# Kernel optimization log

Hardware: AMD Instinct MI355X
Metric: run time of the kernel (lower is better)

## Reference

```python
import jax, jax.numpy as jnp
import numpy as np

OUT = 7           # pooled output size
SR = 2            # sampling_ratio
SCALES = (0.25, 0.125, 0.0625, 0.03125)
K_MIN = 2         # -log2(scales[0])
CANON_SCALE = 224.0
CANON_LVL = 4.0
EPS = 1e-6


def map_levels(boxes):
    # boxes: [N,4] in image coords -> level index in [0, 3]
    area = (boxes[:, 2] - boxes[:, 0]) * (boxes[:, 3] - boxes[:, 1])
    s = jnp.sqrt(area)
    lvl = jnp.floor(CANON_LVL + jnp.log2(s / CANON_SCALE + EPS))
    lvl = jnp.clip(lvl, K_MIN, K_MIN + len(SCALES) - 1)
    return lvl.astype(jnp.int32) - K_MIN


def _sample_coords(lo, bin_sz):
    # sample points within each of OUT bins, SR samples per bin -> [OUT*SR]
    grid = (jnp.arange(OUT, dtype=jnp.float32)[:, None] * bin_sz
            + (jnp.arange(SR, dtype=jnp.float32)[None, :] + 0.5) * bin_sz / SR)
    return lo + grid.reshape(-1)


def _roi_align_single(feat, img, box, scale):
    # feat: [B,C,H,W] (closed over batch under vmap), img: scalar int, box: [4]
    H, W = feat.shape[2], feat.shape[3]
    x1 = box[0] * scale
    y1 = box[1] * scale
    x2 = box[2] * scale
    y2 = box[3] * scale
    roi_w = jnp.maximum(x2 - x1, 1.0)
    roi_h = jnp.maximum(y2 - y1, 1.0)
    ys = _sample_coords(y1, roi_h / OUT)  # [14]
    xs = _sample_coords(x1, roi_w / OUT)  # [14]
    P = OUT * SR
    yg = jnp.broadcast_to(ys[:, None], (P, P)).reshape(-1)  # [196]
    xg = jnp.broadcast_to(xs[None, :], (P, P)).reshape(-1)  # [196]
    # ROIAlign CUDA semantics: out-of-range samples contribute 0
    valid = (yg >= -1.0) & (yg <= H) & (xg >= -1.0) & (xg <= W)
    y = jnp.clip(yg, 0.0, H - 1)
    x = jnp.clip(xg, 0.0, W - 1)
    y0 = jnp.floor(y).astype(jnp.int32)
    x0 = jnp.floor(x).astype(jnp.int32)
    y1i = jnp.minimum(y0 + 1, H - 1)
    x1i = jnp.minimum(x0 + 1, W - 1)
    ly = y - y0
    lx = x - x0
    hy = 1.0 - ly
    hx = 1.0 - lx
    # advanced indices (img, y, x) separated by ':' slice -> result [196, C]
    v00 = feat[img, :, y0, x0]
    v01 = feat[img, :, y0, x1i]
    v10 = feat[img, :, y1i, x0]
    v11 = feat[img, :, y1i, x1i]
    val = ((hy * hx)[:, None] * v00 + (hy * lx)[:, None] * v01
           + (ly * hx)[:, None] * v10 + (ly * lx)[:, None] * v11)
    val = jnp.where(valid[:, None], val, 0.0)
    # [196,C] -> [OUT,SR,OUT,SR,C] -> average over sampling grid -> [OUT,OUT,C]
    val = val.reshape(OUT, SR, OUT, SR, -1).mean(axis=(1, 3))
    return jnp.transpose(val, (2, 0, 1))  # [C,7,7]


def _pooler(feats, boxes, img_ids):
    levels = map_levels(boxes)  # [N]
    N = boxes.shape[0]
    C = feats[0].shape[1]
    result = jnp.zeros((N, C, OUT, OUT), dtype=feats[0].dtype)
    roi_align = jax.vmap(_roi_align_single, in_axes=(None, 0, 0, None))
    for lvl, (feat, scale) in enumerate(zip(feats, SCALES)):
        out_l = roi_align(feat, img_ids, boxes, scale)  # [N,C,7,7]
        result = jnp.where((levels == lvl)[:, None, None, None], out_l, result)
    return result


def setup_inputs() -> dict:
    key = jax.random.key(0)
    ks = jax.random.split(key, 7)
    B, C, N = 2, 256, 1000
    feat0 = jax.random.normal(ks[0], (B, C, 200, 200), jnp.float32)
    feat1 = jax.random.normal(ks[1], (B, C, 100, 100), jnp.float32)
    feat2 = jax.random.normal(ks[2], (B, C, 50, 50), jnp.float32)
    feat3 = jax.random.normal(ks[3], (B, C, 25, 25), jnp.float32)
    # log-uniform box sizes in [16, 400] px spread ROIs across all 4 levels
    wh = jnp.exp(jax.random.uniform(ks[4], (N, 2), minval=jnp.log(16.0),
                                    maxval=jnp.log(400.0)))
    xy = jax.random.uniform(ks[5], (N, 2)) * (800.0 - wh)
    boxes = jnp.concatenate([xy, xy + wh], axis=1)  # [N,4] x1,y1,x2,y2
    img_ids = jax.random.randint(ks[6], (N,), 0, B, dtype=jnp.int32)
    return {"feat0": feat0, "feat1": feat1, "feat2": feat2, "feat3": feat3,
            "boxes": boxes, "img_ids": img_ids}


def reference(feat0, feat1, feat2, feat3, boxes, img_ids):
    return _pooler((feat0, feat1, feat2, feat3), boxes, img_ids)
```

## Files before the change

### kernel.cpp

```cpp
#include <hip/hip_runtime.h>

#define OUTD 7
#define SRD 2
#define PD (OUTD * SRD)
#define NCH 256
#define CHUNK 32

__global__ __launch_bounds__(1024)
void sort_kernel(const float* __restrict__ boxes,
                 const int*   __restrict__ img_ids,
                 int* __restrict__ order, int N)
{
    __shared__ unsigned long long kv[1024];
    const int t = threadIdx.x;

    unsigned int key = 0xFFFFFFFFu;
    if (t < N) {
        const float bx1 = boxes[t * 4 + 0];
        const float by1 = boxes[t * 4 + 1];
        const float bx2 = boxes[t * 4 + 2];
        const float by2 = boxes[t * 4 + 3];
        const float area = (bx2 - bx1) * (by2 - by1);
        const float s = sqrtf(area);
        float lvlf = floorf(4.0f + log2f(s / 224.0f + 1e-6f));
        lvlf = fminf(fmaxf(lvlf, 2.0f), 5.0f);
        const int lvl = (int)lvlf - 2;
        const float scales[4] = {0.25f, 0.125f, 0.0625f, 0.03125f};
        const float sc = scales[lvl];
        int cx = (int)(0.5f * (bx1 + bx2) * sc);
        int cy = (int)(0.5f * (by1 + by2) * sc);
        cx = min(max(cx, 0), 127);
        cy = min(max(cy, 0), 127);
        unsigned int m = 0;
#pragma unroll
        for (int b = 0; b < 7; ++b)
            m |= ((cy >> b) & 1u) << (2 * b + 1) | ((cx >> b) & 1u) << (2 * b);
        key = ((((unsigned)lvl << 1) | (unsigned)img_ids[t]) << 14) | m;
    }
    kv[t] = ((unsigned long long)key << 32) | (unsigned)t;
    __syncthreads();

    for (int k = 2; k <= 1024; k <<= 1) {
        for (int j = k >> 1; j > 0; j >>= 1) {
            const int ixj = t ^ j;
            if (ixj > t) {
                const bool up = ((t & k) == 0);
                const unsigned long long a = kv[t], b = kv[ixj];
                if ((a > b) == up) { kv[t] = b; kv[ixj] = a; }
            }
            __syncthreads();
        }
    }
    if (t < N) order[t] = (int)(kv[t] & 0xFFFFFFFFu);
}

__global__ __launch_bounds__(256)
void pooler_kernel(const float* __restrict__ f0,
                   const float* __restrict__ f1,
                   const float* __restrict__ f2,
                   const float* __restrict__ f3,
                   const float* __restrict__ boxes,
                   const int*   __restrict__ img_ids,
                   const int*   __restrict__ order,
                   float* __restrict__ out, int N)
{
    int bx = blockIdx.x;
    int sidx;
    if ((N & 7) == 0) {
        sidx = (bx & 7) * (N >> 3) + (bx >> 3);
    } else {
        sidx = bx;
    }
    const int roi = order[sidx];

    const int c0  = blockIdx.y * CHUNK;
    const int t   = threadIdx.x;

    const float bx1 = boxes[roi * 4 + 0];
    const float by1 = boxes[roi * 4 + 1];
    const float bx2 = boxes[roi * 4 + 2];
    const float by2 = boxes[roi * 4 + 3];

    const float area = (bx2 - bx1) * (by2 - by1);
    const float s    = sqrtf(area);
    float lvlf = floorf(4.0f + log2f(s / 224.0f + 1e-6f));
    lvlf = fminf(fmaxf(lvlf, 2.0f), 5.0f);
    const int lvl = (int)lvlf - 2;

    const float scales[4] = {0.25f, 0.125f, 0.0625f, 0.03125f};
    const int   dims[4]   = {200, 100, 50, 25};
    const float* feats[4] = {f0, f1, f2, f3};

    const float scale = scales[lvl];
    const int H = dims[lvl];
    const int W = H;
    const int plane = H * W;

    const int img = img_ids[roi];
    const float* __restrict__ base0 =
        feats[lvl] + (size_t)img * NCH * (size_t)plane + (size_t)c0 * plane;

    const float x1 = bx1 * scale, y1 = by1 * scale;
    const float x2 = bx2 * scale, y2 = by2 * scale;
    const float roi_w = fmaxf(x2 - x1, 1.0f);
    const float roi_h = fmaxf(y2 - y1, 1.0f);
    const float bw = roi_w / (float)OUTD;
    const float bh = roi_h / (float)OUTD;

    __shared__ float4 s_yt[PD];
    __shared__ float4 s_xt[PD];
    __shared__ float4 s_xw[OUTD];
    __shared__ int    s_xf[OUTD];
    __shared__ int    s_ok[OUTD];

    if (t < PD) {
        const int i = t >> 1, j = t & 1;
        const float yg = y1 + (float)i * bh + ((float)j + 0.5f) * bh * 0.5f;
        const float v = ((yg >= -1.0f) && (yg <= (float)H)) ? 1.0f : 0.0f;
        const float y = fminf(fmaxf(yg, 0.0f), (float)(H - 1));
        const int y0 = (int)floorf(y);
        const int y1i = min(y0 + 1, H - 1);
        const float ly = y - (float)y0;
        float4 r;
        r.x = __int_as_float(y0 * W);
        r.y = __int_as_float(y1i * W);
        r.z = (1.0f - ly) * v;
        r.w = ly * v;
        s_yt[t] = r;
    } else if (t < 2 * PD) {
        const int tt = t - PD;
        const int i = tt >> 1, j = tt & 1;
        const float xg = x1 + (float)i * bw + ((float)j + 0.5f) * bw * 0.5f;
        const float v = ((xg >= -1.0f) && (xg <= (float)W)) ? 1.0f : 0.0f;
        const float x = fminf(fmaxf(xg, 0.0f), (float)(W - 1));
        const int x0 = (int)floorf(x);
        const float lx = x - (float)x0;
        const float hx = 1.0f - lx;
        const int edge = (x0 == W - 1);
        float4 r;
        r.x = __int_as_float(min(x0, W - 2));
        r.y = edge ? 0.0f   : hx * v;
        r.z = edge ? hx * v : lx * v;
        r.w = 0.0f;
        s_xt[tt] = r;
    } else if (t < 2 * PD + OUTD) {
        const int pw = t - 2 * PD;
        float w[4] = {0.0f, 0.0f, 0.0f, 0.0f};
        int ca[2], cb[2];
        float hxv[2], lxv[2];
#pragma unroll
        for (int j = 0; j < 2; ++j) {
            const float xg = x1 + (float)pw * bw + ((float)j + 0.5f) * bw * 0.5f;
            const float v = ((xg >= -1.0f) && (xg <= (float)W)) ? 1.0f : 0.0f;
            const float x = fminf(fmaxf(xg, 0.0f), (float)(W - 1));
            const int x0 = (int)floorf(x);
            const float lx = x - (float)x0;
            ca[j] = x0;
            cb[j] = min(x0 + 1, W - 1);
            hxv[j] = (1.0f - lx) * v;
            lxv[j] = lx * v;
        }
        const int ok = (cb[1] - ca[0]) <= 3;
        int xf = min(ca[0], W - 4);
        if (xf < 0) xf = 0;
        w[(ca[0] - xf) & 3] += hxv[0];
        w[(cb[0] - xf) & 3] += lxv[0];
        w[(ca[1] - xf) & 3] += hxv[1];
        w[(cb[1] - xf) & 3] += lxv[1];
        float4 wv; wv.x = w[0]; wv.y = w[1]; wv.z = w[2]; wv.w = w[3];
        s_xw[pw] = wv;
        s_xf[pw] = xf;
        s_ok[pw] = ok;
    }
    __syncthreads();

    const bool fused = s_ok[0] && s_ok[1] && s_ok[2] && s_ok[3] &&
                       s_ok[4] && s_ok[5] && s_ok[6];

    float* __restrict__ outbase = out + ((size_t)roi * NCH + c0) * 49;

    if (fused) {
        auto g4 = [&](const float* __restrict__ fp, int ph, int pw, float4* P) {
            const float4 yt0 = s_yt[2 * ph];
            const float4 yt1 = s_yt[2 * ph + 1];
            const int xf = s_xf[pw];
            P[0] = *(const float4*)(fp + __float_as_int(yt0.x) + xf);
            P[1] = *(const float4*)(fp + __float_as_int(yt0.y) + xf);
            P[2] = *(const float4*)(fp + __float_as_int(yt1.x) + xf);
            P[3] = *(const float4*)(fp + __float_as_int(yt1.y) + xf);
        };
        auto r4 = [&](int ph, int pw, const float4* P) -> float {
            const float4 w   = s_xw[pw];
            const float4 yt0 = s_yt[2 * ph];
            const float4 yt1 = s_yt[2 * ph + 1];
            const float d0 = w.x * P[0].x + w.y * P[0].y + w.z * P[0].z + w.w * P[0].w;
            const float d1 = w.x * P[1].x + w.y * P[1].y + w.z * P[1].z + w.w * P[1].w;
            const float d2 = w.x * P[2].x + w.y * P[2].y + w.z * P[2].z + w.w * P[2].w;
            const float d3 = w.x * P[3].x + w.y * P[3].y + w.z * P[3].z + w.w * P[3].w;
            return yt0.z * d0 + yt0.w * d1 + yt1.z * d2 + yt1.w * d3;
        };

        {
            int eA[4], phA[4], pwA[4];
            const float* fpA[4];
#pragma unroll
            for (int j = 0; j < 4; ++j) {
                const int e = t + j * 256;
                const int c = e / 49, bin = e - c * 49;
                phA[j] = bin / 7;
                pwA[j] = bin - phA[j] * 7;
                eA[j]  = e;
                fpA[j] = base0 + (size_t)c * plane;
            }
            float4 P[4][4];
#pragma unroll
            for (int j = 0; j < 4; ++j)
                g4(fpA[j], phA[j], pwA[j], P[j]);
            __builtin_amdgcn_sched_barrier(0);
#pragma unroll
            for (int j = 0; j < 4; ++j)
                outbase[eA[j]] = r4(phA[j], pwA[j], P[j]) * 0.25f;
        }
        {
            int eA[2], phA[2], pwA[2];
            const float* fpA[2];
#pragma unroll
            for (int j = 0; j < 2; ++j) {
                const int e = t + (4 + j) * 256;
                const int c = e / 49, bin = e - c * 49;
                phA[j] = bin / 7;
                pwA[j] = bin - phA[j] * 7;
                eA[j]  = e;
                fpA[j] = base0 + (size_t)c * plane;
            }
            float4 P[2][4];
#pragma unroll
            for (int j = 0; j < 2; ++j)
                g4(fpA[j], phA[j], pwA[j], P[j]);
            __builtin_amdgcn_sched_barrier(0);
#pragma unroll
            for (int j = 0; j < 2; ++j)
                outbase[eA[j]] = r4(phA[j], pwA[j], P[j]) * 0.25f;
        }
        if (t < 32) {
            const int e = 1536 + t;
            const int c = e / 49, bin = e - c * 49;
            const int ph = bin / 7, pw = bin - ph * 7;
            const float* fp = base0 + (size_t)c * plane;
            float4 P[4];
            g4(fp, ph, pw, P);
            outbase[e] = r4(ph, pw, P) * 0.25f;
        }
    } else {
        auto gather = [&](const float* __restrict__ fp, int ph, int pw, float2* P) {
#pragma unroll
            for (int sy = 0; sy < SRD; ++sy) {
                const float4 yt = s_yt[ph * SRD + sy];
                const int ro0 = __float_as_int(yt.x);
                const int ro1 = __float_as_int(yt.y);
#pragma unroll
                for (int sx = 0; sx < SRD; ++sx) {
                    const float4 xt = s_xt[pw * SRD + sx];
                    const int xa = __float_as_int(xt.x);
                    P[(sy * SRD + sx) * 2 + 0] = *(const float2*)(fp + ro0 + xa);
                    P[(sy * SRD + sx) * 2 + 1] = *(const float2*)(fp + ro1 + xa);
                }
            }
        };
        auto reduce = [&](int ph, int pw, const float2* P) -> float {
            float acc = 0.0f;
#pragma unroll
            for (int sy = 0; sy < SRD; ++sy) {
                const float4 yt = s_yt[ph * SRD + sy];
                const float hy = yt.z, ly = yt.w;
#pragma unroll
                for (int sx = 0; sx < SRD; ++sx) {
                    const float4 xt = s_xt[pw * SRD + sx];
                    const float wlo = xt.y, whi = xt.z;
                    const float2 p0 = P[(sy * SRD + sx) * 2 + 0];
                    const float2 p1 = P[(sy * SRD + sx) * 2 + 1];
                    acc += hy * (wlo * p0.x + whi * p0.y)
                         + ly * (wlo * p1.x + whi * p1.y);
                }
            }
            return acc;
        };

#pragma unroll
        for (int kk = 0; kk < 2; ++kk) {
            int eA[3], phA[3], pwA[3];
            const float* fpA[3];
#pragma unroll
            for (int j = 0; j < 3; ++j) {
                const int e = t + (kk * 3 + j) * 256;
                const int c = e / 49, bin = e - c * 49;
                phA[j] = bin / 7;
                pwA[j] = bin - phA[j] * 7;
                eA[j]  = e;
                fpA[j] = base0 + (size_t)c * plane;
            }
            float2 P[3][8];
#pragma unroll
            for (int j = 0; j < 3; ++j)
                gather(fpA[j], phA[j], pwA[j], P[j]);
            __builtin_amdgcn_sched_barrier(0);
#pragma unroll
            for (int j = 0; j < 3; ++j)
                outbase[eA[j]] = reduce(phA[j], pwA[j], P[j]) * 0.25f;
        }
        if (t < 32) {
            const int e = 1536 + t;
            const int c = e / 49, bin = e - c * 49;
            const int ph = bin / 7, pw = bin - ph * 7;
            const float* fp = base0 + (size_t)c * plane;
            float2 P[8];
            gather(fp, ph, pw, P);
            outbase[e] = reduce(ph, pw, P) * 0.25f;
        }
    }
}

extern "C" void kernel_launch(void* const* d_in, const int* in_sizes, int n_in,
                              void* d_out, int out_size, void* d_ws, size_t ws_size,
                              hipStream_t stream) {
    const float* f0    = (const float*)d_in[0];
    const float* f1    = (const float*)d_in[1];
    const float* f2    = (const float*)d_in[2];
    const float* f3    = (const float*)d_in[3];
    const float* boxes = (const float*)d_in[4];
    const int*   ids   = (const int*)d_in[5];
    float* out = (float*)d_out;
    int*   order = (int*)d_ws;

    const int N = in_sizes[4] / 4;

    sort_kernel<<<1, 1024, 0, stream>>>(boxes, ids, order, N);

    dim3 grid(N, NCH / CHUNK);
    pooler_kernel<<<grid, 256, 0, stream>>>(f0, f1, f2, f3, boxes, ids, order, out, N);
}
```

Before: 225.8 us.

## Transpose feature maps to channel-last layout before ROI pooling

```diff
diff --git a/kernel.cpp b/kernel.cpp
--- a/kernel.cpp
+++ b/kernel.cpp
@@ -1,10 +1,15 @@
 #include <hip/hip_runtime.h>
 
 #define OUTD 7
-#define SRD 2
-#define PD (OUTD * SRD)
+#define PD 14
 #define NCH 256
-#define CHUNK 32
+
+#define TOFF0 0
+#define TOFF1 20480000
+#define TOFF2 25600000
+#define TOFF3 26880000
+#define TTOT  27200000
+#define TBASE_BYTES 16384
 
 __global__ __launch_bounds__(1024)
 void sort_kernel(const float* __restrict__ boxes,
@@ -55,7 +60,191 @@
 }
 
 __global__ __launch_bounds__(256)
-void pooler_kernel(const float* __restrict__ f0,
+void transpose_kernel(const float* __restrict__ f0, const float* __restrict__ f1,
+                      const float* __restrict__ f2, const float* __restrict__ f3,
+                      float* __restrict__ T)
+{
+    const int t = threadIdx.x;
+    int id = blockIdx.x;
+    const int ct = id & 3; id >>= 2;
+    const int img = (id >= 832) ? 1 : 0; if (img) id -= 832;
+    int lvl, pt;
+    if (id < 625)      { lvl = 0; pt = id; }
+    else if (id < 782) { lvl = 1; pt = id - 625; }
+    else if (id < 822) { lvl = 2; pt = id - 782; }
+    else               { lvl = 3; pt = id - 822; }
+
+    const int  Ps[4]   = {40000, 10000, 2500, 625};
+    const long TO[4]   = {TOFF0, TOFF1, TOFF2, TOFF3};
+    const float* feats[4] = {f0, f1, f2, f3};
+    const int P = Ps[lvl];
+    const float* __restrict__ src = feats[lvl] + (size_t)img * NCH * (size_t)P;
+    float* __restrict__ dst = T + TO[lvl] + (size_t)img * (size_t)P * NCH;
+    const int p0 = pt * 64, c0 = ct * 64;
+
+    __shared__ float tile[64][65];
+    const int a = t & 15, b = t >> 4;
+
+#pragma unroll
+    for (int i = 0; i < 4; ++i) {
+        const int cs = b + i * 16;
+        const int p4 = a * 4;
+        const float* sp = src + (size_t)(c0 + cs) * P + p0;
+        float4 v;
+        if ((P & 3) == 0 && p0 + p4 + 3 < P) {
+            v = *(const float4*)(sp + p4);
+        } else {
+            const int m = P - 1 - p0;
+            v.x = sp[min(p4 + 0, m)]; v.y = sp[min(p4 + 1, m)];
+            v.z = sp[min(p4 + 2, m)]; v.w = sp[min(p4 + 3, m)];
+        }
+        tile[p4 + 0][cs] = v.x; tile[p4 + 1][cs] = v.y;
+        tile[p4 + 2][cs] = v.z; tile[p4 + 3][cs] = v.w;
+    }
+    __syncthreads();
+#pragma unroll
+    for (int i = 0; i < 4; ++i) {
+        const int ps = b + i * 16;
+        const int c4 = a * 4;
+        if (p0 + ps < P) {
+            float4 v;
+            v.x = tile[ps][c4 + 0]; v.y = tile[ps][c4 + 1];
+            v.z = tile[ps][c4 + 2]; v.w = tile[ps][c4 + 3];
+            *(float4*)(dst + (size_t)(p0 + ps) * NCH + c0 + c4) = v;
+        }
+    }
+}
+
+__global__ __launch_bounds__(256)
+void pooler_t_kernel(const float* __restrict__ T,
+                     const float* __restrict__ boxes,
+                     const int*   __restrict__ img_ids,
+                     const int*   __restrict__ order,
+                     float* __restrict__ out, int N)
+{
+    int bx = blockIdx.x;
+    int sidx;
+    if ((N & 7) == 0) sidx = (bx & 7) * (N >> 3) + (bx >> 3);
+    else              sidx = bx;
+    const int roi = order[sidx];
+    const int t = threadIdx.x;
+
+    const float bx1 = boxes[roi * 4 + 0];
+    const float by1 = boxes[roi * 4 + 1];
+    const float bx2 = boxes[roi * 4 + 2];
+    const float by2 = boxes[roi * 4 + 3];
+
+    const float area = (bx2 - bx1) * (by2 - by1);
+    const float s    = sqrtf(area);
+    float lvlf = floorf(4.0f + log2f(s / 224.0f + 1e-6f));
+    lvlf = fminf(fmaxf(lvlf, 2.0f), 5.0f);
+    const int lvl = (int)lvlf - 2;
+
+    const float scales[4] = {0.25f, 0.125f, 0.0625f, 0.03125f};
+    const int   dims[4]   = {200, 100, 50, 25};
+    const int   Ps[4]     = {40000, 10000, 2500, 625};
+    const long  TO[4]     = {TOFF0, TOFF1, TOFF2, TOFF3};
+
+    const float scale = scales[lvl];
+    const int H = dims[lvl];
+    const int W = H;
+    const int img = img_ids[roi];
+    const float* __restrict__ tb = T + TO[lvl] + (size_t)img * (size_t)Ps[lvl] * NCH;
+
+    const float x1 = bx1 * scale, y1 = by1 * scale;
+    const float x2 = bx2 * scale, y2 = by2 * scale;
+    const float roi_w = fmaxf(x2 - x1, 1.0f);
+    const float roi_h = fmaxf(y2 - y1, 1.0f);
+    const float bw = roi_w / (float)OUTD;
+    const float bh = roi_h / (float)OUTD;
+
+    __shared__ float4 s_yt[PD];
+    __shared__ float4 s_xt[PD];
+    __shared__ float  s_out[49 * 260];
+
+    if (t < PD) {
+        const int i = t >> 1, j = t & 1;
+        const float yg = y1 + (float)i * bh + ((float)j + 0.5f) * bh * 0.5f;
+        const float v = ((yg >= -1.0f) && (yg <= (float)H)) ? 1.0f : 0.0f;
+        const float y = fminf(fmaxf(yg, 0.0f), (float)(H - 1));
+        const int y0 = (int)floorf(y);
+        const int y1i = min(y0 + 1, H - 1);
+        const float ly = y - (float)y0;
+        float4 r;
+        r.x = __int_as_float(y0 * W);
+        r.y = __int_as_float(y1i * W);
+        r.z = (1.0f - ly) * v;
+        r.w = ly * v;
+        s_yt[t] = r;
+    } else if (t < 2 * PD) {
+        const int tt = t - PD;
+        const int i = tt >> 1, j = tt & 1;
+        const float xg = x1 + (float)i * bw + ((float)j + 0.5f) * bw * 0.5f;
+        const float v = ((xg >= -1.0f) && (xg <= (float)W)) ? 1.0f : 0.0f;
+        const float x = fminf(fmaxf(xg, 0.0f), (float)(W - 1));
+        const int x0 = (int)floorf(x);
+        const int x1i = min(x0 + 1, W - 1);
+        const float lx = x - (float)x0;
+        float4 r;
+        r.x = __int_as_float(x0);
+        r.y = __int_as_float(x1i);
+        r.z = (1.0f - lx) * v;
+        r.w = lx * v;
+        s_xt[tt] = r;
+    }
+    __syncthreads();
+
+    const int lane = t & 63;
+    const int w    = t >> 6;
+    const int c4   = lane * 4;
+
+    for (int bin = w; bin < 49; bin += 4) {
+        const int ph = (bin * 37) >> 8;
+        const int pw = bin - ph * 7;
+        float4 acc = {0.0f, 0.0f, 0.0f, 0.0f};
+#pragma unroll
+        for (int sy = 0; sy < 2; ++sy) {
+            const float4 yt = s_yt[ph * 2 + sy];
+            const int r0 = __float_as_int(yt.x);
+            const int r1 = __float_as_int(yt.y);
+            const float hy = yt.z, ly = yt.w;
+#pragma unroll
+            for (int sx = 0; sx < 2; ++sx) {
+                const float4 xt = s_xt[pw * 2 + sx];
+                const int xa = __float_as_int(xt.x);
+                const int xb = __float_as_int(xt.y);
+                const float hx = xt.z, lx = xt.w;
+                const float4 p00 = *(const float4*)(tb + ((size_t)(r0 + xa) << 8) + c4);
+                const float4 p01 = *(const float4*)(tb + ((size_t)(r0 + xb) << 8) + c4);
+                const float4 p10 = *(const float4*)(tb + ((size_t)(r1 + xa) << 8) + c4);
+                const float4 p11 = *(const float4*)(tb + ((size_t)(r1 + xb) << 8) + c4);
+                const float w00 = hy * hx, w01 = hy * lx, w10 = ly * hx, w11 = ly * lx;
+                acc.x += w00 * p00.x + w01 * p01.x + w10 * p10.x + w11 * p11.x;
+                acc.y += w00 * p00.y + w01 * p01.y + w10 * p10.y + w11 * p11.y;
+                acc.z += w00 * p00.z + w01 * p01.z + w10 * p10.z + w11 * p11.z;
+                acc.w += w00 * p00.w + w01 * p01.w + w10 * p10.w + w11 * p11.w;
+            }
+        }
+        float4 r;
+        r.x = acc.x * 0.25f; r.y = acc.y * 0.25f;
+        r.z = acc.z * 0.25f; r.w = acc.w * 0.25f;
+        *(float4*)(&s_out[bin * 260 + c4]) = r;
+    }
+    __syncthreads();
+
+    float* __restrict__ outbase = out + (size_t)roi * (NCH * 49);
+#pragma unroll
+    for (int i = 0; i < 49; ++i) {
+        const int e = t + i * 256;
+        const int c = (int)(((unsigned)e * 21400u) >> 20);
+        const int bin = e - c * 49;
+        outbase[e] = s_out[bin * 260 + c];
+    }
+}
+
+#define LCHUNK 32
+__global__ __launch_bounds__(256)
+void pooler_legacy(const float* __restrict__ f0,
                    const float* __restrict__ f1,
                    const float* __restrict__ f2,
                    const float* __restrict__ f3,
@@ -66,14 +255,11 @@
 {
     int bx = blockIdx.x;
     int sidx;
-    if ((N & 7) == 0) {
-        sidx = (bx & 7) * (N >> 3) + (bx >> 3);
-    } else {
-        sidx = bx;
-    }
+    if ((N & 7) == 0) sidx = (bx & 7) * (N >> 3) + (bx >> 3);
+    else              sidx = bx;
     const int roi = order[sidx];
 
-    const int c0  = blockIdx.y * CHUNK;
+    const int c0  = blockIdx.y * LCHUNK;
     const int t   = threadIdx.x;
 
     const float bx1 = boxes[roi * 4 + 0];
@@ -199,7 +385,6 @@
             const float d3 = w.x * P[3].x + w.y * P[3].y + w.z * P[3].z + w.w * P[3].w;
             return yt0.z * d0 + yt0.w * d1 + yt1.z * d2 + yt1.w * d3;
         };
-
         {
             int eA[4], phA[4], pwA[4];
             const float* fpA[4];
@@ -214,8 +399,7 @@
             }
             float4 P[4][4];
 #pragma unroll
-            for (int j = 0; j < 4; ++j)
-                g4(fpA[j], phA[j], pwA[j], P[j]);
+            for (int j = 0; j < 4; ++j) g4(fpA[j], phA[j], pwA[j], P[j]);
             __builtin_amdgcn_sched_barrier(0);
 #pragma unroll
             for (int j = 0; j < 4; ++j)
@@ -235,8 +419,7 @@
             }
             float4 P[2][4];
 #pragma unroll
-            for (int j = 0; j < 2; ++j)
-                g4(fpA[j], phA[j], pwA[j], P[j]);
+            for (int j = 0; j < 2; ++j) g4(fpA[j], phA[j], pwA[j], P[j]);
             __builtin_amdgcn_sched_barrier(0);
 #pragma unroll
             for (int j = 0; j < 2; ++j)
@@ -254,38 +437,37 @@
     } else {
         auto gather = [&](const float* __restrict__ fp, int ph, int pw, float2* P) {
 #pragma unroll
-            for (int sy = 0; sy < SRD; ++sy) {
-                const float4 yt = s_yt[ph * SRD + sy];
+            for (int sy = 0; sy < 2; ++sy) {
+                const float4 yt = s_yt[ph * 2 + sy];
                 const int ro0 = __float_as_int(yt.x);
                 const int ro1 = __float_as_int(yt.y);
 #pragma unroll
-                for (int sx = 0; sx < SRD; ++sx) {
-                    const float4 xt = s_xt[pw * SRD + sx];
+                for (int sx = 0; sx < 2; ++sx) {
+                    const float4 xt = s_xt[pw * 2 + sx];
                     const int xa = __float_as_int(xt.x);
-                    P[(sy * SRD + sx) * 2 + 0] = *(const float2*)(fp + ro0 + xa);
-                    P[(sy * SRD + sx) * 2 + 1] = *(const float2*)(fp + ro1 + xa);
+                    P[(sy * 2 + sx) * 2 + 0] = *(const float2*)(fp + ro0 + xa);
+                    P[(sy * 2 + sx) * 2 + 1] = *(const float2*)(fp + ro1 + xa);
                 }
             }
         };
         auto reduce = [&](int ph, int pw, const float2* P) -> float {
             float acc = 0.0f;
 #pragma unroll
-            for (int sy = 0; sy < SRD; ++sy) {
-                const float4 yt = s_yt[ph * SRD + sy];
+            for (int sy = 0; sy < 2; ++sy) {
+                const float4 yt = s_yt[ph * 2 + sy];
                 const float hy = yt.z, ly = yt.w;
 #pragma unroll
-                for (int sx = 0; sx < SRD; ++sx) {
-                    const float4 xt = s_xt[pw * SRD + sx];
+                for (int sx = 0; sx < 2; ++sx) {
+                    const float4 xt = s_xt[pw * 2 + sx];
                     const float wlo = xt.y, whi = xt.z;
-                    const float2 p0 = P[(sy * SRD + sx) * 2 + 0];
-                    const float2 p1 = P[(sy * SRD + sx) * 2 + 1];
+                    const float2 p0 = P[(sy * 2 + sx) * 2 + 0];
+                    const float2 p1 = P[(sy * 2 + sx) * 2 + 1];
                     acc += hy * (wlo * p0.x + whi * p0.y)
                          + ly * (wlo * p1.x + whi * p1.y);
                 }
             }
             return acc;
         };
-
 #pragma unroll
         for (int kk = 0; kk < 2; ++kk) {
             int eA[3], phA[3], pwA[3];
@@ -301,8 +483,7 @@
             }
             float2 P[3][8];
 #pragma unroll
-            for (int j = 0; j < 3; ++j)
-                gather(fpA[j], phA[j], pwA[j], P[j]);
+            for (int j = 0; j < 3; ++j) gather(fpA[j], phA[j], pwA[j], P[j]);
             __builtin_amdgcn_sched_barrier(0);
 #pragma unroll
             for (int j = 0; j < 3; ++j)
@@ -334,8 +515,16 @@
 
     const int N = in_sizes[4] / 4;
 
+    const size_t need = (size_t)TBASE_BYTES + (size_t)TTOT * sizeof(float);
+
     sort_kernel<<<1, 1024, 0, stream>>>(boxes, ids, order, N);
 
-    dim3 grid(N, NCH / CHUNK);
-    pooler_kernel<<<grid, 256, 0, stream>>>(f0, f1, f2, f3, boxes, ids, order, out, N);
+    if (ws_size >= need) {
+        float* T = (float*)((char*)d_ws + TBASE_BYTES);
+        transpose_kernel<<<6656, 256, 0, stream>>>(f0, f1, f2, f3, T);
+        pooler_t_kernel<<<N, 256, 0, stream>>>(T, boxes, ids, order, out, N);
+    } else {
+        dim3 grid(N, NCH / LCHUNK);
+        pooler_legacy<<<grid, 256, 0, stream>>>(f0, f1, f2, f3, boxes, ids, order, out, N);
+    }
 }
```

Measured after the change: 231.0 us. 2.3% more time.
